# Kernel tuning notes

Measured on AMD Instinct MI355X. Metric: run time of the kernel, lower is better.

## Reference

```python
import jax, jax.numpy as jnp
import numpy as np

EPS = 1e-5
KW, KH, KER, NF, D, NCLS, NLAYERS = 10, 20, 7, 96, 200, 13, 6
FLAT = NF * (2 * KW - KER + 1) * (KH - KER + 1)  # 96*14*14 = 18816


def _bn(x, g, b, axis):
    # eval-mode batchnorm with running mean 0 / var 1 -> affine with eps correction
    shape = [1] * x.ndim
    shape[axis] = -1
    scale = g * np.float32(1.0 / np.sqrt(1.0 + EPS))
    return x * scale.reshape(shape) + b.reshape(shape)


def _edge_norm(ei, n_nodes):
    # symmetric degree normalization deg^-1/2[src] * deg^-1/2[dst]
    row, col = ei[0], ei[1]
    deg = jnp.zeros((n_nodes,), jnp.float32).at[row].add(1.0)
    dinv = jnp.where(deg > 0, jax.lax.rsqrt(jnp.maximum(deg, 1.0)), 0.0)
    return dinv[row] * dinv[col]


def _forward(node_features, edge_features, inverse_edge_features,
             Win, Wout, Wloop, Wrel, b_gcn,
             bn0_g, bn0_b, conv_w, conv_b, bn1_g, bn1_b,
             fc_w, fc_b, bn2_g, bn2_b, fc1_w, fc1_b,
             edge_index, inverse_edge_index):
    n = node_features.shape[0]
    nf = _edge_norm(edge_index, n)            # [E]
    ni = _edge_norm(inverse_edge_index, n)    # [E]
    x, r, ir = node_features, edge_features, inverse_edge_features
    for l in range(NLAYERS):
        # CompGCN message passing, subtraction composition: comp(x_s, r) = x_s - r
        m_in = ((x[edge_index[0]] - r) @ Win[l]) * nf[:, None]                 # [E, D]
        m_out = ((x[inverse_edge_index[0]] - ir) @ Wout[l]) * ni[:, None]      # [E, D]
        agg = jnp.zeros((n, D), x.dtype)
        agg = agg.at[edge_index[1]].add(m_in)
        agg = agg.at[inverse_edge_index[1]].add(m_out)
        x = jnp.tanh((agg + x @ Wloop[l]) / 3.0 + b_gcn[l])                    # act = tanh
        r = r @ Wrel[l]
        ir = ir @ Wrel[l]
    # ConvE decoder: subject node embedding interleaved with relation embedding
    sub = x[edge_index[0]]                                    # [E, D]
    # cat along dim1 then transpose(2,1).reshape -> elementwise interleave
    stk = jnp.stack([sub, r], axis=-1).reshape(-1, 1, 2 * KW, KH)  # [E,1,20,20]
    h = _bn(stk, bn0_g, bn0_b, 1)
    h = jax.lax.conv_general_dilated(h, conv_w, (1, 1), 'VALID',
                                     dimension_numbers=('NCHW', 'OIHW', 'NCHW'))
    h = h + conv_b[None, :, None, None]                       # [E,96,14,14]
    h = jax.nn.relu(_bn(h, bn1_g, bn1_b, 1))
    h = h.reshape(-1, FLAT)
    h = h @ fc_w.T + fc_b                                     # [E, D]
    h = jax.nn.relu(_bn(h, bn2_g, bn2_b, 1))
    return h @ fc1_w.T + fc1_b                                # [E, NCLS]


def setup_inputs():
    key = jax.random.key(0)
    ks = jax.random.split(key, 16)
    N, E = 5000, 8192
    s = 0.05
    return {
        'node_features': jax.random.normal(ks[0], (N, D), jnp.float32),
        'edge_features': jax.random.normal(ks[1], (E, D), jnp.float32),
        'inverse_edge_features': jax.random.normal(ks[2], (E, D), jnp.float32),
        'Win': jax.random.normal(ks[3], (NLAYERS, D, D), jnp.float32) * s,
        'Wout': jax.random.normal(ks[4], (NLAYERS, D, D), jnp.float32) * s,
        'Wloop': jax.random.normal(ks[5], (NLAYERS, D, D), jnp.float32) * s,
        'Wrel': jax.random.normal(ks[6], (NLAYERS, D, D), jnp.float32) * s,
        'b_gcn': jnp.zeros((NLAYERS, D), jnp.float32),
        'bn0_g': jnp.ones((1,), jnp.float32),
        'bn0_b': jnp.zeros((1,), jnp.float32),
        'conv_w': jax.random.normal(ks[7], (NF, 1, KER, KER), jnp.float32) * s,
        'conv_b': jnp.zeros((NF,), jnp.float32),
        'bn1_g': jnp.ones((NF,), jnp.float32),
        'bn1_b': jnp.zeros((NF,), jnp.float32),
        'fc_w': jax.random.normal(ks[8], (D, FLAT), jnp.float32) * 0.01,
        'fc_b': jnp.zeros((D,), jnp.float32),
        'bn2_g': jnp.ones((D,), jnp.float32),
        'bn2_b': jnp.zeros((D,), jnp.float32),
        'fc1_w': jax.random.normal(ks[9], (NCLS, D), jnp.float32) * s,
        'fc1_b': jnp.zeros((NCLS,), jnp.float32),
        'edge_index': jax.random.randint(ks[10], (2, E), 0, N),
        'inverse_edge_index': jax.random.randint(ks[11], (2, E), 0, N),
    }


def reference(node_features, edge_features, inverse_edge_features, Win, Wout, Wloop, Wrel,
              b_gcn, bn0_g, bn0_b, conv_w, conv_b, bn1_g, bn1_b, fc_w, fc_b,
              bn2_g, bn2_b, fc1_w, fc1_b, edge_index, inverse_edge_index):
    return _forward(node_features, edge_features, inverse_edge_features, Win, Wout, Wloop,
                    Wrel, b_gcn, bn0_g, bn0_b, conv_w, conv_b, bn1_g, bn1_b, fc_w, fc_b,
                    bn2_g, bn2_b, fc1_w, fc1_b, edge_index, inverse_edge_index)
```

## Files before the change

kernel.cpp:

```cpp
#include <hip/hip_runtime.h>
#include <hip/hip_bf16.h>

typedef __hip_bfloat16 bf16;
typedef __attribute__((ext_vector_type(8))) short short8_t;
typedef __attribute__((ext_vector_type(4))) float float4_t;
typedef __attribute__((ext_vector_type(16))) float float16_t;

#define NN 5000
#define EE 8192
#define DM 200
#define NLAY 6
#define NFC 96
#define PPOS 196
#define FLATK 18816
#define NCLS 13
#define EPSC 1e-5f
#define FCRN (7*7*6*64*32*8)

__device__ __forceinline__ float b2f(bf16 v){ return __bfloat162float(v); }
__device__ __forceinline__ float ldf(const void* p, int i, int bf){
  return bf ? b2f(((const bf16*)p)[i]) : ((const float*)p)[i];
}
__device__ __forceinline__ unsigned short f2bu(float f){
  bf16 b = __float2bfloat16(f);
  unsigned short u;
  __builtin_memcpy(&u, &b, 2);
  return u;
}
__device__ __forceinline__ int clampN(int g){ return ((unsigned)g < (unsigned)NN) ? g : 0; }

__global__ void k_dtype(const void* __restrict__ bn1g, int* __restrict__ flag){
  if (blockIdx.x == 0 && threadIdx.x == 0)
    *flag = (*(const unsigned short*)bn1g == 0x3F80u) ? 1 : 0;
}

__global__ void k_cvt(const void* __restrict__ nfeat, const void* __restrict__ ef,
                      const void* __restrict__ ief, float* __restrict__ x0,
                      bf16* __restrict__ r0, bf16* __restrict__ ir0,
                      const int* __restrict__ dtf){
  const int bf = *dtf;
  const int total = NN*DM + 2*EE*DM;
  for (int i = blockIdx.x*blockDim.x + threadIdx.x; i < total; i += gridDim.x*blockDim.x){
    if (i < NN*DM) x0[i] = ldf(nfeat, i, bf);
    else if (i < NN*DM + EE*DM) r0[i - NN*DM] = __float2bfloat16(ldf(ef, i - NN*DM, bf));
    else ir0[i - NN*DM - EE*DM] = __float2bfloat16(ldf(ief, i - NN*DM - EE*DM, bf));
  }
}

__global__ void k_zero(float* __restrict__ p, int n){
  int i = blockIdx.x*blockDim.x + threadIdx.x;
  if (i < n) p[i] = 0.f;
}

__global__ void k_deg(const int* __restrict__ ei0, const int* __restrict__ iei0,
                      float* __restrict__ degf, float* __restrict__ degi){
  int e = blockIdx.x*blockDim.x + threadIdx.x;
  if (e < EE){
    atomicAdd(&degf[clampN(ei0[e])], 1.f);
    atomicAdd(&degi[clampN(iei0[e])], 1.f);
  }
}

__global__ void k_dinv(float* __restrict__ deg2, int n){
  int i = blockIdx.x*blockDim.x + threadIdx.x;
  if (i < n){
    float d = deg2[i];
    deg2[i] = d > 0.f ? rsqrtf(d) : 0.f;
  }
}

__global__ void k_norm(const int* __restrict__ ei, const int* __restrict__ iei,
                       const float* __restrict__ dinvf, const float* __restrict__ dinvi,
                       float* __restrict__ nfv, float* __restrict__ niv){
  int e = blockIdx.x*blockDim.x + threadIdx.x;
  if (e < EE){
    nfv[e] = dinvf[clampN(ei[e])]  * dinvf[clampN(ei[EE + e])];
    niv[e] = dinvi[clampN(iei[e])] * dinvi[clampN(iei[EE + e])];
  }
}

__global__ void k_fcr(const void* __restrict__ fc_w, bf16* __restrict__ outp,
                      const int* __restrict__ dtf){
  const int bf = *dtf;
  int i = blockIdx.x*blockDim.x + threadIdx.x;
  if (i >= FCRN) return;
  int j    = i & 7;
  int row  = (i >> 3) & 31;
  int kch  = (i >> 8) & 63;
  int rest = i >> 14;
  int g = rest % 6;
  int rest2 = rest / 6;
  int pt = rest2 % 7;
  int dgrp = rest2 / 7;
  int d = dgrp*32 + row;
  int cl = kch >> 2, pidx = kch & 3;
  int p = pt*32 + pidx*8 + j;
  int c = g*16 + cl;
  float v = 0.f;
  if (p < PPOS && d < DM) v = ldf(fc_w, d*FLATK + c*PPOS + p, bf);
  outp[i] = __float2bfloat16(v);
}

__global__ void k_wt(const void* __restrict__ Winp, const void* __restrict__ Woutp,
                     const void* __restrict__ Wloopp, const void* __restrict__ Wrelp,
                     bf16* __restrict__ wt, const int* __restrict__ dtf){
  const int bf = *dtf;
  const int per = 6*224*208;
  int i = blockIdx.x*blockDim.x + threadIdx.x;
  if (i >= 4*per) return;
  int job = i / per, rem = i - job*per;
  int layer = rem / (224*208), rem2 = rem - layer*(224*208);
  int n = rem2 / 208, k = rem2 - n*208;
  const void* src = (job==0) ? Wloopp : (job==1) ? Winp : (job==2) ? Woutp : Wrelp;
  float v = 0.f;
  if (n < DM && k < DM) v = ldf(src, (layer*DM + k)*DM + n, bf);
  wt[i] = __float2bfloat16(v);
}

__global__ __launch_bounds__(256) void k_gcn(
    const float* __restrict__ x,
    const bf16* __restrict__ rin, const bf16* __restrict__ irin,
    bf16* __restrict__ rout, bf16* __restrict__ irout,
    const int* __restrict__ ei, const int* __restrict__ iei,
    const float* __restrict__ nfv, const float* __restrict__ niv,
    const bf16* __restrict__ wt, int layer, float* __restrict__ agg)
{
  __shared__ short Ah[32][216];
  __shared__ short Al[32][216];
  __shared__ int dst_s[32];
  const int tid = threadIdx.x;
  const int bid = blockIdx.x;
  int job, m0;
  if (bid < 157){ job = 0; m0 = bid*32; }
  else if (bid < 413){ job = 1; m0 = (bid-157)*32; }
  else if (bid < 669){ job = 2; m0 = (bid-413)*32; }
  else if (bid < 925){ job = 3; m0 = (bid-669)*32; }
  else { job = 4; m0 = (bid-925)*32; }
  const int wsel = (job <= 2) ? job : 3;
  const bf16* W = wt + (wsel*6 + layer)*224*208;
  const bool do_lo = (job <= 2);

  if (tid < 32){
    int row = m0 + tid;
    int d = 0;
    if (job == 1) d = clampN(ei[EE + row]);
    else if (job == 2) d = clampN(iei[EE + row]);
    dst_s[tid] = d;
  }
  for (int t = tid; t < 32*208; t += 256){
    int m = t / 208, k = t - m*208;
    int row = m0 + m;
    float a = 0.f;
    if (k < DM){
      if (job == 0){ if (row < NN) a = x[row*DM + k]; }
      else if (job == 1){ a = (x[clampN(ei[row])*DM + k] - b2f(rin[row*DM + k])) * nfv[row]; }
      else if (job == 2){ a = (x[clampN(iei[row])*DM + k] - b2f(irin[row*DM + k])) * niv[row]; }
      else if (job == 3){ a = b2f(rin[row*DM + k]); }
      else              { a = b2f(irin[row*DM + k]); }
    }
    unsigned short ah = f2bu(a);
    Ah[m][k] = (short)ah;
    if (do_lo){
      float fh = __uint_as_float((unsigned int)ah << 16);
      Al[m][k] = (short)f2bu(a - fh);
    }
  }
  __syncthreads();

  const int lane = tid & 63, wave = tid >> 6;
  const int half = lane >> 5, ln = lane & 31;
  const bool has2 = (wave < 3);
  const bf16* Wn0 = W + (wave*32 + ln)*208;
  const bf16* Wn1 = W + ((wave+4)*32 + ln)*208;
  float16_t acc0 = {};
  float16_t acc1 = {};
  #pragma unroll
  for (int kk = 0; kk < 13; kk++){
    const int ko = kk*16 + half*8;
    short8_t ahf = *(const short8_t*)&Ah[ln][ko];
    short8_t b0 = *(const short8_t*)(Wn0 + ko);
    acc0 = __builtin_amdgcn_mfma_f32_32x32x16_bf16(ahf, b0, acc0, 0, 0, 0);
    short8_t alf = {};
    if (do_lo){
      alf = *(const short8_t*)&Al[ln][ko];
      acc0 = __builtin_amdgcn_mfma_f32_32x32x16_bf16(alf, b0, acc0, 0, 0, 0);
    }
    if (has2){
      short8_t b1 = *(const short8_t*)(Wn1 + ko);
      acc1 = __builtin_amdgcn_mfma_f32_32x32x16_bf16(ahf, b1, acc1, 0, 0, 0);
      if (do_lo)
        acc1 = __builtin_amdgcn_mfma_f32_32x32x16_bf16(alf, b1, acc1, 0, 0, 0);
    }
  }
  #pragma unroll
  for (int s = 0; s < 2; s++){
    if (s == 1 && !has2) break;
    int n = ((s ? wave+4 : wave)*32) + ln;
    if (n >= DM) continue;
    #pragma unroll
    for (int rr = 0; rr < 16; rr++){
      int m = (rr & 3) + 8*(rr >> 2) + 4*half;
      int row = m0 + m;
      float v = s ? acc1[rr] : acc0[rr];
      if (job == 0){ if (row < NN) atomicAdd(&agg[row*DM + n], v); }
      else if (job <= 2){ atomicAdd(&agg[dst_s[m]*DM + n], v); }
      else if (job == 3){ rout[row*DM + n] = __float2bfloat16(v); }
      else              { irout[row*DM + n] = __float2bfloat16(v); }
    }
  }
}

__global__ void k_tanh(float* __restrict__ agg, const void* __restrict__ bgcn,
                       int l, float* __restrict__ xout, const int* __restrict__ dtf){
  const int bf = *dtf;
  int idx = blockIdx.x*blockDim.x + threadIdx.x;
  if (idx < NN*DM){
    int d = idx % DM;
    xout[idx] = tanhf(agg[idx]*(1.f/3.f) + ldf(bgcn, l*DM + d, bf));
    agg[idx] = 0.f;
  }
}

__global__ __launch_bounds__(512) void k_conve(
    const float* __restrict__ xf, const bf16* __restrict__ rf,
    const int* __restrict__ ei0,
    const void* __restrict__ bn0g, const void* __restrict__ bn0b,
    const void* __restrict__ conv_w, const void* __restrict__ conv_b,
    const void* __restrict__ bn1g, const void* __restrict__ bn1b,
    const bf16* __restrict__ fcr, const void* __restrict__ fc_b,
    const void* __restrict__ bn2g, const void* __restrict__ bn2b,
    const void* __restrict__ fc1w, const void* __restrict__ fc1b,
    void* __restrict__ outp, const int* __restrict__ dtf)
{
  const int bfm = *dtf;
  __shared__ __attribute__((aligned(16))) unsigned short img_s[32][400];
  __shared__ __attribute__((aligned(16))) short P_s[3*32*520];
  __shared__ __attribute__((aligned(16))) unsigned short cw_s[96*72];
  __shared__ float bnp_s[3][96];
  const int tid = threadIdx.x;
  const int e0 = blockIdx.x * 32;
  const int lane = tid & 63;
  const int wave = tid >> 6;
  const int half = lane >> 5;
  const int ln   = lane & 31;
  const int m16  = lane & 15;
  const int q4   = (lane >> 4) & 3;

  {
    const float s0 = ldf(bn0g, 0, bfm) * rsqrtf(1.f + EPSC);
    const float c0 = ldf(bn0b, 0, bfm);
    for (int t = tid; t < 32*400; t += 512){
      int me = t / 400, i = t - me*400;
      int e = e0 + me;
      int j = i >> 1;
      float v = (i & 1) ? b2f(rf[e*DM + j]) : xf[clampN(ei0[e])*DM + j];
      img_s[me][i] = f2bu(v * s0 + c0);
    }
    for (int t = tid; t < 96*72; t += 512){
      int c = t / 72, tau = t - c*72;
      float v = (tau < 49) ? ldf(conv_w, c*49 + tau, bfm) : 0.f;
      cw_s[t] = f2bu(v);
    }
    if (tid < 96){
      bnp_s[0][tid] = ldf(bn1g, tid, bfm) * rsqrtf(1.f + EPSC);
      bnp_s[1][tid] = ldf(bn1b, tid, bfm);
      bnp_s[2][tid] = ldf(conv_b, tid, bfm);
    }
  }

  int doff[2][8];
  #pragma unroll
  for (int kk = 0; kk < 2; kk++)
    #pragma unroll
    for (int j = 0; j < 8; j++){
      int tau = kk*32 + q4*8 + j;
      int kh = tau / 7, kw = tau - kh*7;
      doff[kk][j] = (tau < 49) ? kh*20 + kw : 0;
    }

  const int dA0 = wave*32 + ln;
  const bool fcact = (wave < 7);
  float16_t facc = {};

  __syncthreads();

#define FLOAD(BUF, BIDX) { \
    _Pragma("unroll") \
    for (int t_ = 0; t_ < 8; t_++){ \
      int it_ = (BIDX)*8 + t_; \
      int g_ = it_ >> 5; int itm_ = it_ & 31; int kch_ = itm_*2 + half; \
      BUF[t_] = *(const short8_t*)(frW + (g_*64 + kch_)*256 + ln*8); \
    } }
#define FCONS(BUF, BIDX) { \
    _Pragma("unroll") \
    for (int t_ = 0; t_ < 8; t_++){ \
      int it_ = (BIDX)*8 + t_; \
      int g_ = it_ >> 5; int itm_ = it_ & 31; int kch_ = itm_*2 + half; \
      int cl_ = kch_ >> 2, pidx_ = kch_ & 3; \
      short8_t af_ = *(const short8_t*)&P_s[g_*16640 + ln*520 + cl_*32 + ((pidx_ ^ (cl_ & 3))*8)]; \
      facc = __builtin_amdgcn_mfma_f32_32x32x16_bf16(af_, BUF[t_], facc, 0, 0, 0); \
    } }
#define PSTORE(CA, MS) { \
    _Pragma("unroll") \
    for (int r2_ = 0; r2_ < 2; r2_++){ \
      int ploc_ = (MS)*16 + q4*4 + r2_*2; \
      int pg_ = pt*32 + ploc_; \
      float v0_ = ((CA)[r2_*2]   + cbv) * s1v + bb1v;  v0_ = v0_ > 0.f ? v0_ : 0.f; \
      float v1_ = ((CA)[r2_*2+1] + cbv) * s1v + bb1v;  v1_ = v1_ > 0.f ? v1_ : 0.f; \
      if (pg_     >= PPOS) v0_ = 0.f; \
      if (pg_ + 1 >= PPOS) v1_ = 0.f; \
      unsigned int pk_ = (unsigned int)f2bu(v0_) | ((unsigned int)f2bu(v1_) << 16); \
      int sb_ = (ploc_ >> 3) ^ (m16 & 3); \
      *(unsigned int*)&Psec[eL*520 + m16*32 + sb_*8 + (ploc_ & 7)] = pk_; \
    } }

  #pragma unroll 1
  for (int pt = 0; pt < 7; pt++){
    int pbase0, pbase1;
    {
      int p0 = pt*32 + m16;
      int p1 = pt*32 + 16 + m16;
      int oh0 = p0 / 14, ow0 = p0 - oh0*14;
      int oh1 = p1 / 14, ow1 = p1 - oh1*14;
      pbase0 = (p0 < PPOS) ? oh0*20 + ow0 : 0;
      pbase1 = (p1 < PPOS) ? oh1*20 + ow1 : 0;
    }
    #pragma unroll 1
    for (int sub = 0; sub < 2; sub++){
      const bf16* frW = fcr + ((wave*7 + pt)*6 + sub*3)*16384;
      short8_t BbA[8], BbB[8];
      if (fcact) FLOAD(BbA, 0);

      #pragma unroll
      for (int e = 0; e < 4; e++){
        const int eL = wave*4 + e;
        const unsigned short* ib = &img_s[eL][0];
        short8_t A00, A01, A10, A11;
        #pragma unroll
        for (int j = 0; j < 8; j++){
          A00[j] = (short)ib[pbase0 + doff[0][j]];
          A01[j] = (short)ib[pbase0 + doff[1][j]];
          A10[j] = (short)ib[pbase1 + doff[0][j]];
          A11[j] = (short)ib[pbase1 + doff[1][j]];
        }
        #pragma unroll
        for (int g = 0; g < 3; g++){
          const int cidx = (sub*3 + g)*16 + m16;
          short8_t Bg0 = *(const short8_t*)&cw_s[cidx*72 + q4*8];
          short8_t Bg1 = *(const short8_t*)&cw_s[cidx*72 + 32 + q4*8];
          const float s1v  = bnp_s[0][cidx];
          const float bb1v = bnp_s[1][cidx];
          const float cbv  = bnp_s[2][cidx];
          short* Psec = &P_s[g*16640];
          float4_t ca0 = {0.f,0.f,0.f,0.f};
          ca0 = __builtin_amdgcn_mfma_f32_16x16x32_bf16(A00, Bg0, ca0, 0, 0, 0);
          ca0 = __builtin_amdgcn_mfma_f32_16x16x32_bf16(A01, Bg1, ca0, 0, 0, 0);
          PSTORE(ca0, 0);
          float4_t ca1 = {0.f,0.f,0.f,0.f};
          ca1 = __builtin_amdgcn_mfma_f32_16x16x32_bf16(A10, Bg0, ca1, 0, 0, 0);
          ca1 = __builtin_amdgcn_mfma_f32_16x16x32_bf16(A11, Bg1, ca1, 0, 0, 0);
          PSTORE(ca1, 1);
        }
      }
      __syncthreads();
      if (fcact){
        #pragma unroll 1
        for (int bb = 0; bb < 6; bb++){
          const int b0 = bb*2, b1 = bb*2 + 1;
          FLOAD(BbB, b1);
          FCONS(BbA, b0);
          if (bb < 5) FLOAD(BbA, b0 + 2);
          FCONS(BbB, b1);
        }
      }
      __syncthreads();
    }
  }

  float* h2s = (float*)P_s;
  if (fcact && dA0 < DM){
    const float s2  = ldf(bn2g, dA0, bfm) * rsqrtf(1.f + EPSC);
    const float bb2 = ldf(bn2b, dA0, bfm);
    const float fb  = ldf(fc_b, dA0, bfm);
    #pragma unroll
    for (int rr = 0; rr < 16; rr++){
      int m = (rr & 3) + 8*(rr >> 2) + 4*half;
      float v = (facc[rr] + fb) * s2 + bb2;
      h2s[m*201 + dA0] = v > 0.f ? v : 0.f;
    }
  }
  __syncthreads();
  if (tid < 32*NCLS){
    int e = tid / NCLS, n = tid - e*NCLS;
    const float* hr = h2s + e*201;
    float s = ldf(fc1b, n, bfm);
    #pragma unroll 4
    for (int d = 0; d < DM; d++)
      s += hr[d] * ldf(fc1w, n*DM + d, bfm);
    int idx = (e0 + e)*NCLS + n;
    if (bfm) ((bf16*)outp)[idx] = __float2bfloat16(s);
    else     ((float*)outp)[idx] = s;
  }
#undef FLOAD
#undef FCONS
#undef PSTORE
}

extern "C" void kernel_launch(void* const* d_in, const int* in_sizes, int n_in,
                              void* d_out, int out_size, void* d_ws, size_t ws_size,
                              hipStream_t stream){
  const void* nfeat = d_in[0];
  const void* ef    = d_in[1];
  const void* ief   = d_in[2];
  const void* Winp  = d_in[3];
  const void* Woutp = d_in[4];
  const void* Wloopp= d_in[5];
  const void* Wrelp = d_in[6];
  const void* bgcn  = d_in[7];
  const void* bn0g  = d_in[8];
  const void* bn0b  = d_in[9];
  const void* convw = d_in[10];
  const void* convb = d_in[11];
  const void* bn1g  = d_in[12];
  const void* bn1b  = d_in[13];
  const void* fcw   = d_in[14];
  const void* fcb   = d_in[15];
  const void* bn2g  = d_in[16];
  const void* bn2b  = d_in[17];
  const void* fc1w  = d_in[18];
  const void* fc1b  = d_in[19];
  const int* ei     = (const int*)d_in[20];
  const int* iei    = (const int*)d_in[21];

  char* base = (char*)d_ws;
  int*   dtf  = (int*)base;                      base += 16;
  float* x0   = (float*)base;                    base += NN*DM*4;
  float* x1   = (float*)base;                    base += NN*DM*4;
  float* agg  = (float*)base;                    base += NN*DM*4;
  float* degf = (float*)base;                    base += NN*4;
  float* degi = (float*)base;                    base += NN*4;
  float* nfv  = (float*)base;                    base += EE*4;
  float* niv  = (float*)base;                    base += EE*4;
  bf16*  r0   = (bf16*)base;                     base += EE*DM*2;
  bf16*  ir0  = (bf16*)base;                     base += EE*DM*2;
  bf16*  wt   = (bf16*)base;                     base += 4*6*224*208*2;
  bf16*  fcr  = (bf16*)base;                     base += FCRN*2;
  bf16*  rB   = fcr;
  bf16*  irB  = fcr + EE*DM;

  const dim3 B(256);
  k_dtype<<<dim3(1), dim3(64), 0, stream>>>(bn1g, dtf);
  k_cvt<<<dim3(2048), B, 0, stream>>>(nfeat, ef, ief, x0, r0, ir0, dtf);
  k_zero<<<dim3((2*NN + 255)/256), B, 0, stream>>>(degf, 2*NN);
  k_zero<<<dim3((NN*DM + 255)/256), B, 0, stream>>>(agg, NN*DM);
  k_deg<<<dim3((EE + 255)/256), B, 0, stream>>>(ei, iei, degf, degi);
  k_dinv<<<dim3((2*NN + 255)/256), B, 0, stream>>>(degf, 2*NN);
  k_norm<<<dim3((EE + 255)/256), B, 0, stream>>>(ei, iei, degf, degi, nfv, niv);
  k_wt<<<dim3((4*6*224*208 + 255)/256), B, 0, stream>>>(Winp, Woutp, Wloopp, Wrelp, wt, dtf);

  float* xc = x0; float* xn = x1;
  bf16* rc = r0;  bf16* irc = ir0;
  bf16* rn = rB;  bf16* irn = irB;
  for (int l = 0; l < NLAY; l++){
    k_gcn<<<dim3(1181), B, 0, stream>>>(xc, rc, irc, rn, irn, ei, iei, nfv, niv, wt, l, agg);
    k_tanh<<<dim3((NN*DM + 255)/256), B, 0, stream>>>(agg, bgcn, l, xn, dtf);
    float* t = xc; xc = xn; xn = t;
    bf16* tr = rc; rc = rn; rn = tr;
    bf16* ti = irc; irc = irn; irn = ti;
  }
  k_fcr<<<dim3((FCRN + 255)/256), B, 0, stream>>>(fcw, fcr, dtf);
  k_conve<<<dim3(EE/32), dim3(512), 0, stream>>>(xc, rc, ei, bn0g, bn0b,
                                                 convw, convb, bn1g, bn1b,
                                                 fcr, fcb, bn2g, bn2b,
                                                 fc1w, fc1b, d_out, dtf);
}
```

Before: 654.7 us.

## Reorder CompGCN to aggregate-then-multiply and precompute relation weight chain products

Linearity is used to scatter node features per edge first (scaled by the edge norm), then run one fused GEMM per layer. That GEMM takes a concatenated K = [u_in, u_out, x, -S_in, -S_ir] against packed [Win, Wout, Wloop, Q_in, Q_out] weights, and tanh is folded into its epilogue. The relation terms are handled by precomputed chained products of Wrel (Q = P_l·W, with P_l the running product), so the per-layer relation GEMMs disappear and r is transformed once by P6 at the end. This removes the separate tanh/agg-zero pass and the per-edge GEMM work. The cost is per-layer atomic scatter kernels and a low-occupancy 157-block GEMM with K≈1008. The final FC1 loop also gets padded rows and float4 shared-memory loads.

```diff
diff --git a/kernel.cpp b/kernel.cpp
--- a/kernel.cpp
+++ b/kernel.cpp
@@ -16,6 +16,7 @@
 #define NCLS 13
 #define EPSC 1e-5f
 #define FCRN (7*7*6*64*32*8)
+#define BK 1008
 
 __device__ __forceinline__ float b2f(bf16 v){ return __bfloat162float(v); }
 __device__ __forceinline__ float ldf(const void* p, int i, int bf){
@@ -76,6 +77,201 @@
   if (e < EE){
     nfv[e] = dinvf[clampN(ei[e])]  * dinvf[clampN(ei[EE + e])];
     niv[e] = dinvi[clampN(iei[e])] * dinvi[clampN(iei[EE + e])];
+  }
+}
+
+__global__ void k_sS(const bf16* __restrict__ r0, const bf16* __restrict__ ir0,
+                     const int* __restrict__ ei, const int* __restrict__ iei,
+                     const float* __restrict__ nfv, const float* __restrict__ niv,
+                     float* __restrict__ S_in, float* __restrict__ S_ir){
+  int idx = blockIdx.x*blockDim.x + threadIdx.x;
+  const int tot = EE*DM;
+  if (idx < tot){
+    int e = idx / DM, d = idx - e*DM;
+    atomicAdd(&S_in[clampN(ei[EE + e])*DM + d], nfv[e] * b2f(r0[idx]));
+  } else if (idx < 2*tot){
+    int j = idx - tot;
+    int e = j / DM, d = j - e*DM;
+    atomicAdd(&S_ir[clampN(iei[EE + e])*DM + d], niv[e] * b2f(ir0[j]));
+  }
+}
+
+__global__ void k_scat(const float* __restrict__ x,
+                       const int* __restrict__ ei, const int* __restrict__ iei,
+                       const float* __restrict__ nfv, const float* __restrict__ niv,
+                       float* __restrict__ u_in, float* __restrict__ u_out){
+  int idx = blockIdx.x*blockDim.x + threadIdx.x;
+  const int tot = EE*DM;
+  if (idx < tot){
+    int e = idx / DM, d = idx - e*DM;
+    atomicAdd(&u_in[clampN(ei[EE + e])*DM + d], nfv[e] * x[clampN(ei[e])*DM + d]);
+  } else if (idx < 2*tot){
+    int j = idx - tot;
+    int e = j / DM, d = j - e*DM;
+    atomicAdd(&u_out[clampN(iei[EE + e])*DM + d], niv[e] * x[clampN(iei[e])*DM + d]);
+  }
+}
+
+__global__ void k_smm(const void* __restrict__ Winp, const void* __restrict__ Woutp,
+                      const void* __restrict__ Wrelp, const float* __restrict__ Pcur,
+                      int useI, int l, float* __restrict__ Qin, float* __restrict__ Qout,
+                      float* __restrict__ Pnext, const int* __restrict__ dtf){
+  const int bf = *dtf;
+  __shared__ float Prow[DM];
+  int job = blockIdx.x / DM;
+  int r   = blockIdx.x - job*DM;
+  for (int k = threadIdx.x; k < DM; k += blockDim.x)
+    Prow[k] = useI ? (k == r ? 1.f : 0.f) : Pcur[r*DM + k];
+  __syncthreads();
+  const void* W = (job==0) ? Winp : (job==1) ? Woutp : Wrelp;
+  float* out = (job==0) ? Qin : (job==1) ? Qout : Pnext;
+  for (int n = threadIdx.x; n < DM; n += blockDim.x){
+    float acc = 0.f;
+    for (int k = 0; k < DM; k++)
+      acc += Prow[k] * ldf(W, (l*DM + k)*DM + n, bf);
+    out[r*DM + n] = acc;
+  }
+}
+
+__global__ void k_bpack(const void* __restrict__ Winp, const void* __restrict__ Woutp,
+                        const void* __restrict__ Wloopp, const float* __restrict__ Qin,
+                        const float* __restrict__ Qout, bf16* __restrict__ B,
+                        const int* __restrict__ dtf){
+  const int bf = *dtf;
+  const int per = 224*BK;
+  int i = blockIdx.x*blockDim.x + threadIdx.x;
+  if (i >= 6*per) return;
+  int l = i / per, rem = i - l*per;
+  int n = rem / BK, k = rem - n*BK;
+  float v = 0.f;
+  if (n < DM){
+    if (k < 200)       v = ldf(Winp,  (l*DM + k)*DM + n, bf);
+    else if (k < 400)  v = ldf(Woutp, (l*DM + (k-200))*DM + n, bf);
+    else if (k < 600)  v = ldf(Wloopp,(l*DM + (k-400))*DM + n, bf);
+    else if (k < 800)  v = Qin [(l*DM + (k-600))*DM + n];
+    else if (k < 1000) v = Qout[(l*DM + (k-800))*DM + n];
+  }
+  B[i] = __float2bfloat16(v);
+}
+
+__global__ void k_p6t(const float* __restrict__ P6, bf16* __restrict__ out){
+  int i = blockIdx.x*blockDim.x + threadIdx.x;
+  if (i >= 224*208) return;
+  int n = i / 208, k = i - n*208;
+  float v = (n < DM && k < DM) ? P6[k*DM + n] : 0.f;
+  out[i] = __float2bfloat16(v);
+}
+
+__global__ __launch_bounds__(256) void k_rel(bf16* __restrict__ r,
+                                             const bf16* __restrict__ P6t){
+  __shared__ short Ah[32][216];
+  const int tid = threadIdx.x;
+  const int m0 = blockIdx.x*32;
+  for (int t = tid; t < 32*208; t += 256){
+    int m = t / 208, k = t - m*208;
+    Ah[m][k] = (k < DM) ? (short)((const unsigned short*)r)[(m0+m)*DM + k] : (short)0;
+  }
+  __syncthreads();
+  const int lane = tid & 63, wave = tid >> 6;
+  const int half = lane >> 5, ln = lane & 31;
+  const bool has2 = (wave < 3);
+  const bf16* Wn0 = P6t + (wave*32 + ln)*208;
+  const bf16* Wn1 = P6t + ((wave+4)*32 + ln)*208;
+  float16_t acc0 = {}, acc1 = {};
+  #pragma unroll
+  for (int kk = 0; kk < 13; kk++){
+    const int ko = kk*16 + half*8;
+    short8_t ahf = *(const short8_t*)&Ah[ln][ko];
+    short8_t b0 = *(const short8_t*)(Wn0 + ko);
+    acc0 = __builtin_amdgcn_mfma_f32_32x32x16_bf16(ahf, b0, acc0, 0, 0, 0);
+    if (has2){
+      short8_t b1 = *(const short8_t*)(Wn1 + ko);
+      acc1 = __builtin_amdgcn_mfma_f32_32x32x16_bf16(ahf, b1, acc1, 0, 0, 0);
+    }
+  }
+  __syncthreads();
+  #pragma unroll
+  for (int s = 0; s < 2; s++){
+    if (s == 1 && !has2) break;
+    int n = ((s ? wave+4 : wave)*32) + ln;
+    if (n >= DM) continue;
+    #pragma unroll
+    for (int rr = 0; rr < 16; rr++){
+      int m = (rr & 3) + 8*(rr >> 2) + 4*half;
+      float v = s ? acc1[rr] : acc0[rr];
+      r[(m0 + m)*DM + n] = __float2bfloat16(v);
+    }
+  }
+}
+
+__global__ __launch_bounds__(256) void k_gemm(
+    const float* __restrict__ x, const float* __restrict__ u_in,
+    const float* __restrict__ u_out, const float* __restrict__ S_in,
+    const float* __restrict__ S_ir, const bf16* __restrict__ B, int layer,
+    const void* __restrict__ bgcn, float* __restrict__ xout,
+    const int* __restrict__ dtf)
+{
+  const int bf = *dtf;
+  __shared__ short Ah[32][1016];
+  __shared__ short Al[32][1016];
+  const int tid = threadIdx.x;
+  const int m0 = blockIdx.x*32;
+  #pragma unroll 1
+  for (int m = 0; m < 32; m++){
+    int row = m0 + m;
+    bool ok = row < NN;
+    for (int k = tid; k < BK; k += 256){
+      float a = 0.f;
+      if (ok){
+        if (k < 200)       a = u_in [row*DM + k];
+        else if (k < 400)  a = u_out[row*DM + (k-200)];
+        else if (k < 600)  a = x    [row*DM + (k-400)];
+        else if (k < 800)  a = -S_in[row*DM + (k-600)];
+        else if (k < 1000) a = -S_ir[row*DM + (k-800)];
+      }
+      unsigned short ah = f2bu(a);
+      Ah[m][k] = (short)ah;
+      float fh = __uint_as_float((unsigned int)ah << 16);
+      Al[m][k] = (short)f2bu(a - fh);
+    }
+  }
+  __syncthreads();
+
+  const int lane = tid & 63, wave = tid >> 6;
+  const int half = lane >> 5, ln = lane & 31;
+  const bool has2 = (wave < 3);
+  const bf16* Bl = B + layer*224*BK;
+  const bf16* Wn0 = Bl + (wave*32 + ln)*BK;
+  const bf16* Wn1 = Bl + ((wave+4)*32 + ln)*BK;
+  float16_t acc0 = {}, acc1 = {};
+  for (int kk = 0; kk < BK/16; kk++){
+    const int ko = kk*16 + half*8;
+    short8_t ahf = *(const short8_t*)&Ah[ln][ko];
+    short8_t alf = *(const short8_t*)&Al[ln][ko];
+    short8_t b0 = *(const short8_t*)(Wn0 + ko);
+    acc0 = __builtin_amdgcn_mfma_f32_32x32x16_bf16(ahf, b0, acc0, 0, 0, 0);
+    acc0 = __builtin_amdgcn_mfma_f32_32x32x16_bf16(alf, b0, acc0, 0, 0, 0);
+    if (has2){
+      short8_t b1 = *(const short8_t*)(Wn1 + ko);
+      acc1 = __builtin_amdgcn_mfma_f32_32x32x16_bf16(ahf, b1, acc1, 0, 0, 0);
+      acc1 = __builtin_amdgcn_mfma_f32_32x32x16_bf16(alf, b1, acc1, 0, 0, 0);
+    }
+  }
+  #pragma unroll
+  for (int s = 0; s < 2; s++){
+    if (s == 1 && !has2) break;
+    int n = ((s ? wave+4 : wave)*32) + ln;
+    if (n >= DM) continue;
+    const float bv = ldf(bgcn, layer*DM + n, bf);
+    #pragma unroll
+    for (int rr = 0; rr < 16; rr++){
+      int m = (rr & 3) + 8*(rr >> 2) + 4*half;
+      int row = m0 + m;
+      if (row < NN){
+        float v = s ? acc1[rr] : acc0[rr];
+        xout[row*DM + n] = tanhf(v*(1.f/3.f) + bv);
+      }
+    }
   }
 }
 
@@ -99,126 +295,6 @@
   float v = 0.f;
   if (p < PPOS && d < DM) v = ldf(fc_w, d*FLATK + c*PPOS + p, bf);
   outp[i] = __float2bfloat16(v);
-}
-
-__global__ void k_wt(const void* __restrict__ Winp, const void* __restrict__ Woutp,
-                     const void* __restrict__ Wloopp, const void* __restrict__ Wrelp,
-                     bf16* __restrict__ wt, const int* __restrict__ dtf){
-  const int bf = *dtf;
-  const int per = 6*224*208;
-  int i = blockIdx.x*blockDim.x + threadIdx.x;
-  if (i >= 4*per) return;
-  int job = i / per, rem = i - job*per;
-  int layer = rem / (224*208), rem2 = rem - layer*(224*208);
-  int n = rem2 / 208, k = rem2 - n*208;
-  const void* src = (job==0) ? Wloopp : (job==1) ? Winp : (job==2) ? Woutp : Wrelp;
-  float v = 0.f;
-  if (n < DM && k < DM) v = ldf(src, (layer*DM + k)*DM + n, bf);
-  wt[i] = __float2bfloat16(v);
-}
-
-__global__ __launch_bounds__(256) void k_gcn(
-    const float* __restrict__ x,
-    const bf16* __restrict__ rin, const bf16* __restrict__ irin,
-    bf16* __restrict__ rout, bf16* __restrict__ irout,
-    const int* __restrict__ ei, const int* __restrict__ iei,
-    const float* __restrict__ nfv, const float* __restrict__ niv,
-    const bf16* __restrict__ wt, int layer, float* __restrict__ agg)
-{
-  __shared__ short Ah[32][216];
-  __shared__ short Al[32][216];
-  __shared__ int dst_s[32];
-  const int tid = threadIdx.x;
-  const int bid = blockIdx.x;
-  int job, m0;
-  if (bid < 157){ job = 0; m0 = bid*32; }
-  else if (bid < 413){ job = 1; m0 = (bid-157)*32; }
-  else if (bid < 669){ job = 2; m0 = (bid-413)*32; }
-  else if (bid < 925){ job = 3; m0 = (bid-669)*32; }
-  else { job = 4; m0 = (bid-925)*32; }
-  const int wsel = (job <= 2) ? job : 3;
-  const bf16* W = wt + (wsel*6 + layer)*224*208;
-  const bool do_lo = (job <= 2);
-
-  if (tid < 32){
-    int row = m0 + tid;
-    int d = 0;
-    if (job == 1) d = clampN(ei[EE + row]);
-    else if (job == 2) d = clampN(iei[EE + row]);
-    dst_s[tid] = d;
-  }
-  for (int t = tid; t < 32*208; t += 256){
-    int m = t / 208, k = t - m*208;
-    int row = m0 + m;
-    float a = 0.f;
-    if (k < DM){
-      if (job == 0){ if (row < NN) a = x[row*DM + k]; }
-      else if (job == 1){ a = (x[clampN(ei[row])*DM + k] - b2f(rin[row*DM + k])) * nfv[row]; }
-      else if (job == 2){ a = (x[clampN(iei[row])*DM + k] - b2f(irin[row*DM + k])) * niv[row]; }
-      else if (job == 3){ a = b2f(rin[row*DM + k]); }
-      else              { a = b2f(irin[row*DM + k]); }
-    }
-    unsigned short ah = f2bu(a);
-    Ah[m][k] = (short)ah;
-    if (do_lo){
-      float fh = __uint_as_float((unsigned int)ah << 16);
-      Al[m][k] = (short)f2bu(a - fh);
-    }
-  }
-  __syncthreads();
-
-  const int lane = tid & 63, wave = tid >> 6;
-  const int half = lane >> 5, ln = lane & 31;
-  const bool has2 = (wave < 3);
-  const bf16* Wn0 = W + (wave*32 + ln)*208;
-  const bf16* Wn1 = W + ((wave+4)*32 + ln)*208;
-  float16_t acc0 = {};
-  float16_t acc1 = {};
-  #pragma unroll
-  for (int kk = 0; kk < 13; kk++){
-    const int ko = kk*16 + half*8;
-    short8_t ahf = *(const short8_t*)&Ah[ln][ko];
-    short8_t b0 = *(const short8_t*)(Wn0 + ko);
-    acc0 = __builtin_amdgcn_mfma_f32_32x32x16_bf16(ahf, b0, acc0, 0, 0, 0);
-    short8_t alf = {};
-    if (do_lo){
-      alf = *(const short8_t*)&Al[ln][ko];
-      acc0 = __builtin_amdgcn_mfma_f32_32x32x16_bf16(alf, b0, acc0, 0, 0, 0);
-    }
-    if (has2){
-      short8_t b1 = *(const short8_t*)(Wn1 + ko);
-      acc1 = __builtin_amdgcn_mfma_f32_32x32x16_bf16(ahf, b1, acc1, 0, 0, 0);
-      if (do_lo)
-        acc1 = __builtin_amdgcn_mfma_f32_32x32x16_bf16(alf, b1, acc1, 0, 0, 0);
-    }
-  }
-  #pragma unroll
-  for (int s = 0; s < 2; s++){
-    if (s == 1 && !has2) break;
-    int n = ((s ? wave+4 : wave)*32) + ln;
-    if (n >= DM) continue;
-    #pragma unroll
-    for (int rr = 0; rr < 16; rr++){
-      int m = (rr & 3) + 8*(rr >> 2) + 4*half;
-      int row = m0 + m;
-      float v = s ? acc1[rr] : acc0[rr];
-      if (job == 0){ if (row < NN) atomicAdd(&agg[row*DM + n], v); }
-      else if (job <= 2){ atomicAdd(&agg[dst_s[m]*DM + n], v); }
-      else if (job == 3){ rout[row*DM + n] = __float2bfloat16(v); }
-      else              { irout[row*DM + n] = __float2bfloat16(v); }
-    }
-  }
-}
-
-__global__ void k_tanh(float* __restrict__ agg, const void* __restrict__ bgcn,
-                       int l, float* __restrict__ xout, const int* __restrict__ dtf){
-  const int bf = *dtf;
-  int idx = blockIdx.x*blockDim.x + threadIdx.x;
-  if (idx < NN*DM){
-    int d = idx % DM;
-    xout[idx] = tanhf(agg[idx]*(1.f/3.f) + ldf(bgcn, l*DM + d, bf));
-    agg[idx] = 0.f;
-  }
 }
 
 __global__ __launch_bounds__(512) void k_conve(
@@ -311,7 +387,7 @@
       if (pg_ + 1 >= PPOS) v1_ = 0.f; \
       unsigned int pk_ = (unsigned int)f2bu(v0_) | ((unsigned int)f2bu(v1_) << 16); \
       int sb_ = (ploc_ >> 3) ^ (m16 & 3); \
-      *(unsigned int*)&Psec[eL*520 + m16*32 + sb_*8 + (ploc_ & 7)] = pk_; \
+      *(unsigned int*)&P_s[(g)*16640 + eL*520 + m16*32 + sb_*8 + (ploc_ & 7)] = pk_; \
     } }
 
   #pragma unroll 1
@@ -351,7 +427,6 @@
           const float s1v  = bnp_s[0][cidx];
           const float bb1v = bnp_s[1][cidx];
           const float cbv  = bnp_s[2][cidx];
-          short* Psec = &P_s[g*16640];
           float4_t ca0 = {0.f,0.f,0.f,0.f};
           ca0 = __builtin_amdgcn_mfma_f32_16x16x32_bf16(A00, Bg0, ca0, 0, 0, 0);
           ca0 = __builtin_amdgcn_mfma_f32_16x16x32_bf16(A01, Bg1, ca0, 0, 0, 0);
@@ -386,17 +461,23 @@
     for (int rr = 0; rr < 16; rr++){
       int m = (rr & 3) + 8*(rr >> 2) + 4*half;
       float v = (facc[rr] + fb) * s2 + bb2;
-      h2s[m*201 + dA0] = v > 0.f ? v : 0.f;
+      h2s[m*204 + dA0] = v > 0.f ? v : 0.f;
     }
   }
   __syncthreads();
   if (tid < 32*NCLS){
     int e = tid / NCLS, n = tid - e*NCLS;
-    const float* hr = h2s + e*201;
+    const float4* h4p = (const float4*)(h2s + e*204);
     float s = ldf(fc1b, n, bfm);
-    #pragma unroll 4
-    for (int d = 0; d < DM; d++)
-      s += hr[d] * ldf(fc1w, n*DM + d, bfm);
+    #pragma unroll 2
+    for (int d4 = 0; d4 < 50; d4++){
+      float4 h4 = h4p[d4];
+      int d = d4*4;
+      s += h4.x * ldf(fc1w, n*DM + d, bfm);
+      s += h4.y * ldf(fc1w, n*DM + d + 1, bfm);
+      s += h4.z * ldf(fc1w, n*DM + d + 2, bfm);
+      s += h4.w * ldf(fc1w, n*DM + d + 3, bfm);
+    }
     int idx = (e0 + e)*NCLS + n;
     if (bfm) ((bf16*)outp)[idx] = __float2bfloat16(s);
     else     ((float*)outp)[idx] = s;
@@ -436,40 +517,54 @@
   int*   dtf  = (int*)base;                      base += 16;
   float* x0   = (float*)base;                    base += NN*DM*4;
   float* x1   = (float*)base;                    base += NN*DM*4;
-  float* agg  = (float*)base;                    base += NN*DM*4;
+  float* S_in = (float*)base;                    base += NN*DM*4;
+  float* S_ir = (float*)base;                    base += NN*DM*4;
   float* degf = (float*)base;                    base += NN*4;
   float* degi = (float*)base;                    base += NN*4;
   float* nfv  = (float*)base;                    base += EE*4;
   float* niv  = (float*)base;                    base += EE*4;
   bf16*  r0   = (bf16*)base;                     base += EE*DM*2;
   bf16*  ir0  = (bf16*)base;                     base += EE*DM*2;
-  bf16*  wt   = (bf16*)base;                     base += 4*6*224*208*2;
+  bf16*  Bp   = (bf16*)base;                     base += 6*224*BK*2;
   bf16*  fcr  = (bf16*)base;                     base += FCRN*2;
-  bf16*  rB   = fcr;
-  bf16*  irB  = fcr + EE*DM;
+  float* u_in  = (float*)fcr;
+  float* u_out = u_in + NN*DM;
+  float* Pa   = x1;
+  float* Pb   = x1 + 40000;
+  float* Qin  = x1 + 80000;
+  float* Qout = x1 + 320000;
+  bf16*  P6t  = (bf16*)(x1 + 560000);
 
   const dim3 B(256);
   k_dtype<<<dim3(1), dim3(64), 0, stream>>>(bn1g, dtf);
   k_cvt<<<dim3(2048), B, 0, stream>>>(nfeat, ef, ief, x0, r0, ir0, dtf);
   k_zero<<<dim3((2*NN + 255)/256), B, 0, stream>>>(degf, 2*NN);
-  k_zero<<<dim3((NN*DM + 255)/256), B, 0, stream>>>(agg, NN*DM);
   k_deg<<<dim3((EE + 255)/256), B, 0, stream>>>(ei, iei, degf, degi);
   k_dinv<<<dim3((2*NN + 255)/256), B, 0, stream>>>(degf, 2*NN);
   k_norm<<<dim3((EE + 255)/256), B, 0, stream>>>(ei, iei, degf, degi, nfv, niv);
-  k_wt<<<dim3((4*6*224*208 + 255)/256), B, 0, stream>>>(Winp, Woutp, Wloopp, Wrelp, wt, dtf);
+
+  k_zero<<<dim3((2*NN*DM + 255)/256), B, 0, stream>>>(S_in, 2*NN*DM);
+  k_sS<<<dim3((2*EE*DM + 255)/256), B, 0, stream>>>(r0, ir0, ei, iei, nfv, niv, S_in, S_ir);
+
+  float* Pc = Pa; float* Pn = Pb;
+  for (int l = 0; l < NLAY; l++){
+    k_smm<<<dim3(3*DM), B, 0, stream>>>(Winp, Woutp, Wrelp, Pc, (l==0)?1:0, l,
+                                        Qin + l*DM*DM, Qout + l*DM*DM, Pn, dtf);
+    float* t = Pc; Pc = Pn; Pn = t;
+  }
+  k_bpack<<<dim3((6*224*BK + 255)/256), B, 0, stream>>>(Winp, Woutp, Wloopp, Qin, Qout, Bp, dtf);
+  k_p6t<<<dim3((224*208 + 255)/256), B, 0, stream>>>(Pc, P6t);
+  k_rel<<<dim3(EE/32), B, 0, stream>>>(r0, P6t);
 
   float* xc = x0; float* xn = x1;
-  bf16* rc = r0;  bf16* irc = ir0;
-  bf16* rn = rB;  bf16* irn = irB;
   for (int l = 0; l < NLAY; l++){
-    k_gcn<<<dim3(1181), B, 0, stream>>>(xc, rc, irc, rn, irn, ei, iei, nfv, niv, wt, l, agg);
-    k_tanh<<<dim3((NN*DM + 255)/256), B, 0, stream>>>(agg, bgcn, l, xn, dtf);
+    k_zero<<<dim3((2*NN*DM + 255)/256), B, 0, stream>>>(u_in, 2*NN*DM);
+    k_scat<<<dim3((2*EE*DM + 255)/256), B, 0, stream>>>(xc, ei, iei, nfv, niv, u_in, u_out);
+    k_gemm<<<dim3(157), B, 0, stream>>>(xc, u_in, u_out, S_in, S_ir, Bp, l, bgcn, xn, dtf);
     float* t = xc; xc = xn; xn = t;
-    bf16* tr = rc; rc = rn; rn = tr;
-    bf16* ti = irc; irc = irn; irn = ti;
   }
   k_fcr<<<dim3((FCRN + 255)/256), B, 0, stream>>>(fcw, fcr, dtf);
-  k_conve<<<dim3(EE/32), dim3(512), 0, stream>>>(xc, rc, ei, bn0g, bn0b,
+  k_conve<<<dim3(EE/32), dim3(512), 0, stream>>>(xc, r0, ei, bn0g, bn0b,
                                                  convw, convb, bn1g, bn1b,
                                                  fcr, fcb, bn2g, bn2b,
                                                  fc1w, fc1b, d_out, dtf);
```

Result: slower. 1.224 ms (+86.9%).
